# Kernel optimization log

Hardware: AMD Instinct MI355X
Metric: run time of the kernel (lower is better)

## Reference

```python
import jax, jax.numpy as jnp
import numpy as np

D_MODEL = 40; N_LAYER = 256
D_INNER = 80; D_STATE = 16; D_CONV = 4; DT_RANK = 3  # mamba defaults: expand=2, dt_rank=ceil(40/16)
PE_HID = 48; FF_MULT = 4
B, L, N = 1, 400, 65536


def setup_inputs():
    key = jax.random.key(0)
    ks = jax.random.split(key, 16)
    f32 = jnp.float32
    def rn(k, shape, s=0.02):
        return jax.random.normal(k, shape, f32) * s
    inp = {}
    inp['mash_params'] = jax.random.normal(ks[0], (B, L, D_MODEL), f32)
    inp['qry'] = jax.random.uniform(ks[1], (B, N, 3), f32, -1.0, 1.0)
    # stacked per-layer Mamba params (leading dim = N_LAYER)
    inp['l_norm_w'] = jnp.ones((N_LAYER, D_MODEL), f32)
    inp['l_in_w'] = rn(ks[2], (N_LAYER, 2 * D_INNER, D_MODEL), 0.05)
    inp['l_conv_w'] = rn(ks[3], (N_LAYER, D_INNER, D_CONV), 0.2)
    inp['l_conv_b'] = jnp.zeros((N_LAYER, D_INNER), f32)
    inp['l_xproj_w'] = rn(ks[4], (N_LAYER, DT_RANK + 2 * D_STATE, D_INNER), 0.05)
    inp['l_dt_w'] = rn(ks[5], (N_LAYER, D_INNER, DT_RANK), 0.2)
    inp['l_dt_b'] = rn(ks[6], (N_LAYER, D_INNER), 0.5) - 4.0  # softplus -> small dt
    A = jnp.tile(jnp.arange(1, D_STATE + 1, dtype=f32)[None, None, :], (N_LAYER, D_INNER, 1))
    inp['l_A_log'] = jnp.log(A)
    inp['l_D'] = jnp.ones((N_LAYER, D_INNER), f32)
    inp['l_out_w'] = rn(ks[7], (N_LAYER, D_MODEL, D_INNER), 0.05)
    # PointEmbed MLP (Fourier basis is a fixed buffer, built in forward)
    inp['pe_mlp_w'] = rn(ks[8], (D_MODEL, PE_HID + 3), 0.1)
    inp['pe_mlp_b'] = jnp.zeros((D_MODEL,), f32)
    # PreNorm cross-attention (heads=1, dim_head=d_model)
    inp['ca_lnq_w'] = jnp.ones((D_MODEL,), f32); inp['ca_lnq_b'] = jnp.zeros((D_MODEL,), f32)
    inp['ca_lnc_w'] = jnp.ones((D_MODEL,), f32); inp['ca_lnc_b'] = jnp.zeros((D_MODEL,), f32)
    inp['ca_q_w'] = rn(ks[9], (D_MODEL, D_MODEL), 0.1)
    inp['ca_kv_w'] = rn(ks[10], (2 * D_MODEL, D_MODEL), 0.1)
    inp['ca_out_w'] = rn(ks[11], (D_MODEL, D_MODEL), 0.1)
    inp['ca_out_b'] = jnp.zeros((D_MODEL,), f32)
    # PreNorm GEGLU feed-forward
    inp['ff_ln_w'] = jnp.ones((D_MODEL,), f32); inp['ff_ln_b'] = jnp.zeros((D_MODEL,), f32)
    inp['ff_fc1_w'] = rn(ks[12], (2 * FF_MULT * D_MODEL, D_MODEL), 0.1)
    inp['ff_fc1_b'] = jnp.zeros((2 * FF_MULT * D_MODEL,), f32)
    inp['ff_fc2_w'] = rn(ks[13], (D_MODEL, FF_MULT * D_MODEL), 0.1)
    inp['ff_fc2_b'] = jnp.zeros((D_MODEL,), f32)
    inp['out_w'] = rn(ks[14], (1, D_MODEL), 0.1)
    inp['out_b'] = jnp.zeros((1,), f32)
    return inp


def _rmsnorm(x, w, eps=1e-5):
    return x * jax.lax.rsqrt(jnp.mean(x * x, -1, keepdims=True) + eps) * w


def _layernorm(x, w, b, eps=1e-5):
    m = jnp.mean(x, -1, keepdims=True)
    v = jnp.mean((x - m) ** 2, -1, keepdims=True)
    return (x - m) * jax.lax.rsqrt(v + eps) * w + b


def _mamba(u, p):
    # u: [b, l, d_model]
    xz = jnp.einsum('bld,ed->ble', u, p['in_w'])  # [b,l,2*di]
    x, z = jnp.split(xz, 2, -1)
    # depthwise causal conv1d, kernel D_CONV
    xt = jnp.swapaxes(x, 1, 2)  # [b, di, l]
    xc = jax.lax.conv_general_dilated(xt, p['conv_w'][:, None, :], (1,), [(D_CONV - 1, 0)],
                                      feature_group_count=D_INNER)
    x = jax.nn.silu(jnp.swapaxes(xc + p['conv_b'][None, :, None], 1, 2))  # [b,l,di]
    dbc = jnp.einsum('bld,ed->ble', x, p['xproj_w'])  # [b,l,dt_rank+2*ds]
    dtr = dbc[..., :DT_RANK]
    Bm = dbc[..., DT_RANK:DT_RANK + D_STATE]
    Cm = dbc[..., DT_RANK + D_STATE:]
    dt = jax.nn.softplus(jnp.einsum('blr,dr->bld', dtr, p['dt_w']) + p['dt_b'])  # [b,l,di]
    A = -jnp.exp(p['A_log'])  # [di, ds]
    dA = jnp.exp(dt[..., None] * A)                          # [b,l,di,ds]
    dBx = dt[..., None] * Bm[:, :, None, :] * x[..., None]   # [b,l,di,ds]
    def step(h, io):
        a, bx = io
        h = a * h + bx
        return h, h
    h0 = jnp.zeros((u.shape[0], D_INNER, D_STATE), u.dtype)
    _, hs = jax.lax.scan(step, h0, (jnp.moveaxis(dA, 1, 0), jnp.moveaxis(dBx, 1, 0)))
    hs = jnp.moveaxis(hs, 0, 1)  # [b,l,di,ds]
    y = jnp.einsum('blds,bls->bld', hs, Cm) + x * p['D']
    y = y * jax.nn.silu(z)
    return jnp.einsum('bld,ed->ble', y, p['out_w'])


def _forward(mash_params, qry, l_norm_w, l_in_w, l_conv_w, l_conv_b, l_xproj_w, l_dt_w, l_dt_b,
             l_A_log, l_D, l_out_w, pe_mlp_w, pe_mlp_b, ca_lnq_w, ca_lnq_b, ca_lnc_w, ca_lnc_b,
             ca_q_w, ca_kv_w, ca_out_w, ca_out_b, ff_ln_w, ff_ln_b, ff_fc1_w, ff_fc1_b,
             ff_fc2_w, ff_fc2_b, out_w, out_b):
    layer_params = dict(norm_w=l_norm_w, in_w=l_in_w, conv_w=l_conv_w, conv_b=l_conv_b,
                        xproj_w=l_xproj_w, dt_w=l_dt_w, dt_b=l_dt_b, A_log=l_A_log,
                        D=l_D, out_w=l_out_w)
    # Block: residual = x; h = RMSNorm(x); h = Mamba(h); then caller does x = h + residual
    def layer_fn(x, p):
        return x + _mamba(_rmsnorm(x, p['norm_w']), p), None
    x, _ = jax.lax.scan(layer_fn, mash_params, layer_params)
    # PointEmbed: Fourier features with fixed block-diagonal basis
    e = (2.0 ** jnp.arange(PE_HID // 6, dtype=jnp.float32)) * jnp.pi  # [8]
    z0 = jnp.zeros_like(e)
    basis = jnp.stack([jnp.concatenate([e, z0, z0]),
                       jnp.concatenate([z0, e, z0]),
                       jnp.concatenate([z0, z0, e])])  # [3, 24]
    proj = jnp.einsum('bnd,de->bne', qry, basis)
    pe = jnp.concatenate([jnp.sin(proj), jnp.cos(proj), qry], -1)  # [b,n,51]
    q_emb = jnp.einsum('bnf,df->bnd', pe, pe_mlp_w) + pe_mlp_b
    # PreNorm cross-attention (1 head, dim_head = d_model)
    qn = _layernorm(q_emb, ca_lnq_w, ca_lnq_b)
    cn = _layernorm(x, ca_lnc_w, ca_lnc_b)
    q = jnp.einsum('bnd,ed->bne', qn, ca_q_w)
    kv = jnp.einsum('bld,ed->ble', cn, ca_kv_w)
    k, v = jnp.split(kv, 2, -1)
    scale = D_MODEL ** -0.5
    attn = jax.nn.softmax(jnp.einsum('bnd,bld->bnl', q, k) * scale, axis=-1)  # [b,n,l]
    lat = jnp.einsum('bnl,bld->bnd', attn, v)
    lat = jnp.einsum('bnd,ed->bne', lat, ca_out_w) + ca_out_b
    # PreNorm GEGLU feed-forward with residual
    h = _layernorm(lat, ff_ln_w, ff_ln_b)
    a = jnp.einsum('bnd,ed->bne', h, ff_fc1_w) + ff_fc1_b
    x1, g = jnp.split(a, 2, -1)
    ff = jnp.einsum('bnf,df->bnd', x1 * jax.nn.gelu(g, approximate=False), ff_fc2_w) + ff_fc2_b
    lat = lat + ff
    occ = (jnp.einsum('bnd,od->bno', lat, out_w) + out_b)[..., 0]  # [b, n]
    return occ


def reference(mash_params, qry, l_norm_w, l_in_w, l_conv_w, l_conv_b, l_xproj_w, l_dt_w, l_dt_b,
              l_A_log, l_D, l_out_w, pe_mlp_w, pe_mlp_b, ca_lnq_w, ca_lnq_b, ca_lnc_w, ca_lnc_b,
              ca_q_w, ca_kv_w, ca_out_w, ca_out_b, ff_ln_w, ff_ln_b, ff_fc1_w, ff_fc1_b,
              ff_fc2_w, ff_fc2_b, out_w, out_b):
    return _forward(mash_params, qry, l_norm_w, l_in_w, l_conv_w, l_conv_b, l_xproj_w, l_dt_w,
                    l_dt_b, l_A_log, l_D, l_out_w, pe_mlp_w, pe_mlp_b, ca_lnq_w, ca_lnq_b,
                    ca_lnc_w, ca_lnc_b, ca_q_w, ca_kv_w, ca_out_w, ca_out_b, ff_ln_w, ff_ln_b,
                    ff_fc1_w, ff_fc1_b, ff_fc2_w, ff_fc2_b, out_w, out_b)
```

## Files before the change

kernel.cpp:

```cpp
#include <hip/hip_runtime.h>


#define CH 4
#define NCHUNK 100
#define TPB1 320

typedef unsigned long long u64;

__device__ __forceinline__ u64 pack2(float a, float b) {
  return ((u64)__float_as_uint(b) << 32) | (u64)__float_as_uint(a);
}
__device__ __forceinline__ float unplo(u64 a) {
  return __uint_as_float((unsigned)a);
}
__device__ __forceinline__ float unphi(u64 a) {
  return __uint_as_float((unsigned)(a >> 32));
}

__global__ void init_flags(int* __restrict__ flags) {
  int i = blockIdx.x * 256 + threadIdx.x;
  if (i < 256 * 16) flags[i] = 0;
}

__global__ __launch_bounds__(TPB1) void mamba_pipe(
    const float* __restrict__ mash,
    const float* __restrict__ g_norm_w,
    const float* __restrict__ g_in_w,
    const float* __restrict__ g_conv_w,
    const float* __restrict__ g_conv_b,
    const float* __restrict__ g_xp_w,
    const float* __restrict__ g_dt_w,
    const float* __restrict__ g_dt_b,
    const float* __restrict__ g_alog,
    const float* __restrict__ g_D,
    const float* __restrict__ g_out_w,
    float* __restrict__ xb0,
    float* __restrict__ xb1,
    int* __restrict__ flags,
    const float* __restrict__ qry,
    const float* __restrict__ pe_w, const float* __restrict__ pe_b,
    const float* __restrict__ lnq_w, const float* __restrict__ lnq_b,
    const float* __restrict__ qw,
    float* __restrict__ qstore)
{
  const int tid = threadIdx.x;

  if (blockIdx.x >= 256) {
    const int n = (blockIdx.x - 256) * TPB1 + tid;
    if (n < 65536) {
      const float qx = qry[n * 3 + 0], qy = qry[n * 3 + 1], qz = qry[n * 3 + 2];
      float qe[40];
#pragma unroll
      for (int d = 0; d < 40; ++d) qe[d] = pe_b[d];
#pragma unroll 1
      for (int j = 0; j < 8; ++j) {
        float f = 3.14159265358979323846f * (float)(1 << j);
        float sx, cx, sy, cy, sz, cz;
        __sincosf(qx * f, &sx, &cx);
        __sincosf(qy * f, &sy, &cy);
        __sincosf(qz * f, &sz, &cz);
#pragma unroll
        for (int d = 0; d < 40; ++d) {
          const float* r = pe_w + d * 51;
          qe[d] += sx * r[j] + sy * r[j + 8] + sz * r[j + 16]
                 + cx * r[j + 24] + cy * r[j + 32] + cz * r[j + 40];
        }
      }
#pragma unroll
      for (int d = 0; d < 40; ++d) {
        const float* r = pe_w + d * 51;
        qe[d] += qx * r[48] + qy * r[49] + qz * r[50];
      }
      float qn[40];
      {
        float m = 0.f;
#pragma unroll
        for (int d = 0; d < 40; ++d) m += qe[d];
        m *= (1.f / 40.f);
        float var = 0.f;
#pragma unroll
        for (int d = 0; d < 40; ++d) { float dv = qe[d] - m; var += dv * dv; }
        float rstd = rsqrtf(var * (1.f / 40.f) + 1e-5f);
#pragma unroll
        for (int d = 0; d < 40; ++d)
          qn[d] = (qe[d] - m) * rstd * lnq_w[d] + lnq_b[d];
      }
      float q[40];
#pragma unroll
      for (int e = 0; e < 40; ++e) {
        const float* r = qw + e * 40;
        float s = 0.f;
#pragma unroll
        for (int d = 0; d < 40; ++d) s += qn[d] * r[d];
        q[e] = s;
      }
#pragma unroll
      for (int e = 0; e < 40; ++e) qstore[e * 65536 + n] = q[e];
    }
    return;
  }

  const int layer = blockIdx.x;

  __shared__ float xin[160];
  __shared__ float xz[640];
  __shared__ float xs[320];
  __shared__ float dbc[144];
  __shared__ float yb[320];
  __shared__ float xhist[240];

  const int e_in = tid % 160;
  const int tA = tid / 160;
  float w_in_r[40];
  {
    const float4* g = (const float4*)(g_in_w + layer * 6400 + e_in * 40);
    const float4* nw = (const float4*)(g_norm_w + layer * 40);
#pragma unroll
    for (int k = 0; k < 10; ++k) {
      float4 v = g[k];
      float4 n = nw[k];
      w_in_r[4 * k] = v.x * n.x; w_in_r[4 * k + 1] = v.y * n.y;
      w_in_r[4 * k + 2] = v.z * n.z; w_in_r[4 * k + 3] = v.w * n.w;
    }
  }
  const int d_c = tid % 80;
  const int t_c = tid / 80;
  float cw[4]; float cb;
  {
    float4 v = *(const float4*)(g_conv_w + layer * 320 + d_c * 4);
    cw[0] = v.x; cw[1] = v.y; cw[2] = v.z; cw[3] = v.w;
    cb = g_conv_b[layer * 80 + d_c];
  }
  const int halfp = tid & 1;
  const int p_x = tid >> 1;
  const int t_x = p_x / 35, e_x = p_x % 35;
  float w_xp_r[40];
  if (p_x < 140) {
    const float4* g = (const float4*)(g_xp_w + layer * 2800 + e_x * 80 + halfp * 40);
#pragma unroll
    for (int k = 0; k < 10; ++k) {
      float4 v = g[k];
      w_xp_r[4 * k] = v.x; w_xp_r[4 * k + 1] = v.y;
      w_xp_r[4 * k + 2] = v.z; w_xp_r[4 * k + 3] = v.w;
    }
  }
  const int d_ch = tid >> 2;
  const int qq = tid & 3;
  float negA[4], hst[4];
  {
    float4 v = *(const float4*)(g_alog + layer * 1280 + tid * 4);
    negA[0] = -__expf(v.x); negA[1] = -__expf(v.y);
    negA[2] = -__expf(v.z); negA[3] = -__expf(v.w);
    hst[0] = hst[1] = hst[2] = hst[3] = 0.f;
  }
  const float dtw0 = g_dt_w[layer * 240 + d_ch * 3 + 0];
  const float dtw1 = g_dt_w[layer * 240 + d_ch * 3 + 1];
  const float dtw2 = g_dt_w[layer * 240 + d_ch * 3 + 2];
  const float dtb = g_dt_b[layer * 80 + d_ch];
  const float wD = g_D[layer * 80 + d_ch];
  const int p_o = tid >> 1;
  const int t_o = p_o / 40, e_o = p_o % 40;
  float w_out_r[40];
  {
    const float4* g = (const float4*)(g_out_w + layer * 3200 + e_o * 80 + halfp * 40);
#pragma unroll
    for (int k = 0; k < 10; ++k) {
      float4 v = g[k];
      w_out_r[4 * k] = v.x; w_out_r[4 * k + 1] = v.y;
      w_out_r[4 * k + 2] = v.z; w_out_r[4 * k + 3] = v.w;
    }
  }

  for (int i = tid; i < 240; i += TPB1) xhist[i] = 0.f;
  __syncthreads();

  const float* src = (layer == 0) ? mash : ((layer & 1) ? xb0 : xb1);
  float* dst = (layer & 1) ? xb1 : xb0;
  int* flag_prev = flags + (layer - 1) * 16;
  int* flag_cur = flags + layer * 16;

  for (int c = 0; c < NCHUNK; ++c) {
    const int t0 = c * CH;

    if (layer == 0) {
#pragma unroll
      for (int tt = 0; tt < 2; ++tt) {
        const int t = tA + 2 * tt;
        const float4* sp = (const float4*)(src + (t0 + t) * 40);
        float ss = 0.f, sd = 0.f;
#pragma unroll
        for (int k = 0; k < 10; ++k) {
          float4 v = sp[k];
          ss += v.x * v.x + v.y * v.y + v.z * v.z + v.w * v.w;
          sd += w_in_r[4 * k] * v.x + w_in_r[4 * k + 1] * v.y
              + w_in_r[4 * k + 2] * v.z + w_in_r[4 * k + 3] * v.w;
        }
        xz[t * 160 + e_in] = sd * rsqrtf(ss * (1.f / 40.f) + 1e-5f);
      }
      if (tid < 160) xin[tid] = src[t0 * 40 + tid];
    } else {
      while (__hip_atomic_load(flag_prev, __ATOMIC_RELAXED,
                               __HIP_MEMORY_SCOPE_AGENT) <= c)
        __builtin_amdgcn_s_sleep(1);
#pragma unroll
      for (int tt = 0; tt < 2; ++tt) {
        const int t = tA + 2 * tt;
        const u64* sp = (const u64*)(src + (t0 + t) * 40);
        float ss = 0.f, sd = 0.f;
#pragma unroll
        for (int k = 0; k < 20; ++k) {
          u64 a = __hip_atomic_load(sp + k, __ATOMIC_RELAXED,
                                    __HIP_MEMORY_SCOPE_AGENT);
          float v0 = unplo(a), v1 = unphi(a);
          ss += v0 * v0 + v1 * v1;
          sd += w_in_r[2 * k] * v0 + w_in_r[2 * k + 1] * v1;
        }
        xz[t * 160 + e_in] = sd * rsqrtf(ss * (1.f / 40.f) + 1e-5f);
      }
      if (tid < 80) {
        u64 a = __hip_atomic_load((const u64*)(src + t0 * 40) + tid,
                                  __ATOMIC_RELAXED, __HIP_MEMORY_SCOPE_AGENT);
        xin[2 * tid] = unplo(a);
        xin[2 * tid + 1] = unphi(a);
      }
    }
    __syncthreads();

    {
      float acc = cb;
#pragma unroll
      for (int j = 0; j < 4; ++j) {
        int lt = t_c - 3 + j;
        float xv = (lt >= 0) ? xz[lt * 160 + d_c] : xhist[(lt + 3) * 80 + d_c];
        acc += cw[j] * xv;
      }
      xs[t_c * 80 + d_c] = acc / (1.f + __expf(-acc));
    }
    __syncthreads();

    if (p_x < 140) {
      const float4* xp = (const float4*)&xs[t_x * 80 + halfp * 40];
      float s = 0.f;
#pragma unroll
      for (int k = 0; k < 10; ++k) {
        float4 v = xp[k];
        s += w_xp_r[4 * k] * v.x + w_xp_r[4 * k + 1] * v.y
           + w_xp_r[4 * k + 2] * v.z + w_xp_r[4 * k + 3] * v.w;
      }
      s += __shfl_xor(s, 1);
      if (halfp == 0) dbc[t_x * 36 + e_x] = s;
    } else {
      for (int k = tid - 280; k < 240; k += 40)
        xhist[k] = xz[(1 + k / 80) * 160 + (k % 80)];
    }
    __syncthreads();

#pragma unroll
    for (int t = 0; t < CH; ++t) {
      const float* db = &dbc[t * 36];
      float sdt = dtb + db[0] * dtw0 + db[1] * dtw1 + db[2] * dtw2;
      float dtval = (sdt > 15.f) ? sdt : __logf(1.f + __expf(sdt));
      float xval = xs[t * 80 + d_ch];
      float part = 0.f;
#pragma unroll
      for (int j = 0; j < 4; ++j) {
        int s_i = qq * 4 + j;
        float Bv = db[3 + s_i];
        float Cv = db[19 + s_i];
        hst[j] = __expf(dtval * negA[j]) * hst[j] + dtval * Bv * xval;
        part += hst[j] * Cv;
      }
      part += __shfl_xor(part, 1);
      part += __shfl_xor(part, 2);
      if (qq == 0) {
        float yv = part + xval * wD;
        float z = xz[t * 160 + 80 + d_ch];
        yb[t * 80 + d_ch] = yv * z / (1.f + __expf(-z));
      }
    }
    __syncthreads();

    {
      const float4* yp = (const float4*)&yb[t_o * 80 + halfp * 40];
      float s = 0.f;
#pragma unroll
      for (int k = 0; k < 10; ++k) {
        float4 v = yp[k];
        s += w_out_r[4 * k] * v.x + w_out_r[4 * k + 1] * v.y
           + w_out_r[4 * k + 2] * v.z + w_out_r[4 * k + 3] * v.w;
      }
      s += __shfl_xor(s, 1);
      float r = xin[p_o] + s;
      float r2 = __shfl_xor(r, 2);
      if ((tid & 3) == 0)
        __hip_atomic_store((u64*)(dst + t0 * 40 + p_o), pack2(r, r2),
                           __ATOMIC_RELAXED, __HIP_MEMORY_SCOPE_AGENT);
    }
    __syncthreads();
    if (tid == 0)
      __hip_atomic_store(flag_cur, c + 1, __ATOMIC_RELAXED,
                         __HIP_MEMORY_SCOPE_AGENT);
  }
}

__global__ __launch_bounds__(64) void kv_kernel(
    const float* __restrict__ xfin,
    const float* __restrict__ lnc_w, const float* __restrict__ lnc_b,
    const float* __restrict__ kv_w,
    float* __restrict__ kbuf, float* __restrict__ vbuf)
{
  int t = blockIdx.x;
  int lane = threadIdx.x;
  float x = (lane < 40) ? xfin[t * 40 + lane] : 0.f;
  float s = x;
#pragma unroll
  for (int o = 32; o >= 1; o >>= 1) s += __shfl_xor(s, o);
  float m = s * (1.f / 40.f);
  float dv = (lane < 40) ? (x - m) : 0.f;
  float v2 = dv * dv;
#pragma unroll
  for (int o = 32; o >= 1; o >>= 1) v2 += __shfl_xor(v2, o);
  float rstd = rsqrtf(v2 * (1.f / 40.f) + 1e-5f);
  __shared__ float cn[40];
  if (lane < 40) cn[lane] = dv * rstd * lnc_w[lane] + lnc_b[lane];
  __syncthreads();
  for (int e = lane; e < 80; e += 64) {
    float acc = 0.f;
#pragma unroll
    for (int d = 0; d < 40; ++d) acc += cn[d] * kv_w[e * 40 + d];
    if (e < 40) kbuf[t * 40 + e] = acc;
    else vbuf[t * 40 + (e - 40)] = acc;
  }
}

__global__ __launch_bounds__(256) void query_fast(
    const float* __restrict__ qstore,
    const float* __restrict__ ow, const float* __restrict__ ob,
    const float* __restrict__ flw, const float* __restrict__ flb,
    const float* __restrict__ w1, const float* __restrict__ b1,
    const float* __restrict__ w2, const float* __restrict__ b2,
    const float* __restrict__ outw, const float* __restrict__ outb,
    const float* __restrict__ kbuf, const float* __restrict__ vbuf,
    float* __restrict__ out)
{
  const int tid = threadIdx.x;
  const int h = __builtin_amdgcn_readfirstlane((tid >> 6) & 3);
  const int lane = tid & 63;
  const int n = blockIdx.x * 64 + lane;
  const int p1 = tid ^ 64, p2 = tid ^ 128, p3 = tid ^ 192;
  __shared__ float colbuf[40 * 256];

  float q[40];
#pragma unroll
  for (int e = 0; e < 40; ++e) q[e] = qstore[e * 65536 + n];

  float acc[40];
#pragma unroll
  for (int d = 0; d < 40; ++d) acc[d] = 0.f;
  float mx = -1e30f, l = 0.f;
  const float scale = 0.15811388300841897f;
  const int tbeg = h * 100;
#pragma unroll 1
  for (int t = tbeg; t < tbeg + 100; t += 2) {
    const float4* ka = (const float4*)(kbuf + t * 40);
    const float4* kb = (const float4*)(kbuf + t * 40 + 40);
    float a0 = 0.f, a1 = 0.f, b0 = 0.f, b1s = 0.f;
#pragma unroll
    for (int k = 0; k < 10; ++k) {
      float4 k4 = ka[k];
      float4 j4 = kb[k];
      a0 += q[4 * k] * k4.x + q[4 * k + 1] * k4.y;
      a1 += q[4 * k + 2] * k4.z + q[4 * k + 3] * k4.w;
      b0 += q[4 * k] * j4.x + q[4 * k + 1] * j4.y;
      b1s += q[4 * k + 2] * j4.z + q[4 * k + 3] * j4.w;
    }
    float sa = (a0 + a1) * scale;
    float sb = (b0 + b1s) * scale;
    {
      if (sa > mx) {
        float corr = __expf(mx - sa);
        l *= corr;
#pragma unroll
        for (int d = 0; d < 40; ++d) acc[d] *= corr;
        mx = sa;
      }
      float p = __expf(sa - mx);
      l += p;
      const float4* vr = (const float4*)(vbuf + t * 40);
#pragma unroll
      for (int k = 0; k < 10; ++k) {
        float4 v4 = vr[k];
        acc[4 * k] += p * v4.x; acc[4 * k + 1] += p * v4.y;
        acc[4 * k + 2] += p * v4.z; acc[4 * k + 3] += p * v4.w;
      }
    }
    {
      if (sb > mx) {
        float corr = __expf(mx - sb);
        l *= corr;
#pragma unroll
        for (int d = 0; d < 40; ++d) acc[d] *= corr;
        mx = sb;
      }
      float p = __expf(sb - mx);
      l += p;
      const float4* vr = (const float4*)(vbuf + (t + 1) * 40);
#pragma unroll
      for (int k = 0; k < 10; ++k) {
        float4 v4 = vr[k];
        acc[4 * k] += p * v4.x; acc[4 * k + 1] += p * v4.y;
        acc[4 * k + 2] += p * v4.z; acc[4 * k + 3] += p * v4.w;
      }
    }
  }

  {
    float* redm = colbuf;
    float* redl = colbuf + 256;
    redm[tid] = mx; redl[tid] = l;
  }
  __syncthreads();
  float a0c, a1c, a2c, a3c, linv;
  {
    float m1 = colbuf[p1], m2 = colbuf[p2], m3 = colbuf[p3];
    float l1 = colbuf[256 + p1], l2 = colbuf[256 + p2], l3 = colbuf[256 + p3];
    float nm = fmaxf(fmaxf(mx, m1), fmaxf(m2, m3));
    a0c = __expf(mx - nm); a1c = __expf(m1 - nm);
    a2c = __expf(m2 - nm); a3c = __expf(m3 - nm);
    float L = l * a0c + l1 * a1c + l2 * a2c + l3 * a3c;
    linv = 1.f / L;
  }
  __syncthreads();
#pragma unroll
  for (int d = 0; d < 40; ++d) colbuf[d * 256 + tid] = acc[d];
  __syncthreads();
  float lat[40];
#pragma unroll
  for (int d = 0; d < 40; ++d)
    lat[d] = (acc[d] * a0c + colbuf[d * 256 + p1] * a1c
            + colbuf[d * 256 + p2] * a2c + colbuf[d * 256 + p3] * a3c) * linv;
  __syncthreads();

  float lath[10];
#pragma unroll
  for (int dd = 0; dd < 10; ++dd) {
    float v = lat[dd];
    v = (h == 1) ? lat[dd + 10] : v;
    v = (h == 2) ? lat[dd + 20] : v;
    v = (h == 3) ? lat[dd + 30] : v;
    lath[dd] = v;
  }
  float lp[40];
#pragma unroll
  for (int e = 0; e < 40; ++e) lp[e] = 0.f;
#pragma unroll 1
  for (int dd = 0; dd < 10; ++dd) {
    const float lv = lath[dd];
    const int d = h * 10 + dd;
#pragma unroll
    for (int e = 0; e < 40; ++e) lp[e] += lv * ow[e * 40 + d];
  }
#pragma unroll
  for (int e = 0; e < 40; ++e) colbuf[e * 256 + tid] = lp[e];
  __syncthreads();
  float lat2[40];
#pragma unroll
  for (int e = 0; e < 40; ++e)
    lat2[e] = ob[e] + lp[e] + colbuf[e * 256 + p1]
            + colbuf[e * 256 + p2] + colbuf[e * 256 + p3];
  __syncthreads();

  float hh[40];
  {
    float m = 0.f;
#pragma unroll
    for (int d = 0; d < 40; ++d) m += lat2[d];
    m *= (1.f / 40.f);
    float var = 0.f;
#pragma unroll
    for (int d = 0; d < 40; ++d) { float dv = lat2[d] - m; var += dv * dv; }
    float rstd = rsqrtf(var * (1.f / 40.f) + 1e-5f);
#pragma unroll
    for (int d = 0; d < 40; ++d) hh[d] = (lat2[d] - m) * rstd * flw[d] + flb[d];
  }
  float ff[40];
#pragma unroll
  for (int d = 0; d < 40; ++d) ff[d] = 0.f;
#pragma unroll 1
  for (int ee = 0; ee < 40; ++ee) {
    const int e = h * 40 + ee;
    const float* r1 = w1 + e * 40;
    const float* r2 = w1 + (160 + e) * 40;
    float s0 = 0.f, s1 = 0.f;
#pragma unroll
    for (int d = 0; d < 40; ++d) { s0 += hh[d] * r1[d]; s1 += hh[d] * r2[d]; }
    float x1 = s0 + b1[e];
    float g = s1 + b1[160 + e];
    float tv = x1 * (0.5f * g * (1.f + erff(g * 0.70710678118654752f)));
#pragma unroll
    for (int d = 0; d < 40; ++d) ff[d] += tv * w2[d * 160 + e];
  }
#pragma unroll
  for (int d = 0; d < 40; ++d) colbuf[d * 256 + tid] = ff[d];
  __syncthreads();
  float r = outb[0];
#pragma unroll
  for (int d = 0; d < 40; ++d) {
    float f = ff[d] + colbuf[d * 256 + p1] + colbuf[d * 256 + p2]
            + colbuf[d * 256 + p3] + b2[d];
    r += (lat2[d] + f) * outw[d];
  }
  if (h == 0) out[n] = r;
}

__global__ __launch_bounds__(256) void query_kernel_fb(
    const float* __restrict__ qry,
    const float* __restrict__ pe_w, const float* __restrict__ pe_b,
    const float* __restrict__ lnq_w, const float* __restrict__ lnq_b,
    const float* __restrict__ qw,
    const float* __restrict__ ow, const float* __restrict__ ob,
    const float* __restrict__ flw, const float* __restrict__ flb,
    const float* __restrict__ w1, const float* __restrict__ b1,
    const float* __restrict__ w2, const float* __restrict__ b2,
    const float* __restrict__ outw, const float* __restrict__ outb,
    const float* __restrict__ kbuf, const float* __restrict__ vbuf,
    float* __restrict__ out)
{
  const int tid = threadIdx.x;
  const int h = __builtin_amdgcn_readfirstlane((tid >> 6) & 1);
  const int pj = tid >> 7;
  const int lane = tid & 63;
  const int n = blockIdx.x * 128 + pj * 64 + lane;
  const int ptn = tid ^ 64;
  __shared__ float colbuf[40 * 256];
  __shared__ float redm[256], redl[256];

  const float qx = qry[n * 3 + 0], qy = qry[n * 3 + 1], qz = qry[n * 3 + 2];
  float qp[40];
#pragma unroll
  for (int d = 0; d < 40; ++d) qp[d] = 0.f;
#pragma unroll
  for (int jj = 0; jj < 4; ++jj) {
    const int j = h * 4 + jj;
    float f = 3.14159265358979323846f * (float)(1 << j);
    float sx, cx, sy, cy, sz, cz;
    __sincosf(qx * f, &sx, &cx);
    __sincosf(qy * f, &sy, &cy);
    __sincosf(qz * f, &sz, &cz);
#pragma unroll
    for (int d = 0; d < 40; ++d) {
      const float* r = pe_w + d * 51;
      qp[d] += sx * r[j] + sy * r[j + 8] + sz * r[j + 16]
             + cx * r[j + 24] + cy * r[j + 32] + cz * r[j + 40];
    }
  }
#pragma unroll
  for (int d = 0; d < 40; ++d) colbuf[d * 256 + tid] = qp[d];
  __syncthreads();
  float qe[40];
#pragma unroll
  for (int d = 0; d < 40; ++d) {
    const float* r = pe_w + d * 51;
    qe[d] = pe_b[d] + qp[d] + colbuf[d * 256 + ptn]
          + qx * r[48] + qy * r[49] + qz * r[50];
  }
  __syncthreads();
  float qn[40];
  {
    float m = 0.f;
#pragma unroll
    for (int d = 0; d < 40; ++d) m += qe[d];
    m *= (1.f / 40.f);
    float var = 0.f;
#pragma unroll
    for (int d = 0; d < 40; ++d) { float dv = qe[d] - m; var += dv * dv; }
    float rstd = rsqrtf(var * (1.f / 40.f) + 1e-5f);
#pragma unroll
    for (int d = 0; d < 40; ++d) qn[d] = (qe[d] - m) * rstd * lnq_w[d] + lnq_b[d];
  }
  float qnh[20];
#pragma unroll
  for (int dd = 0; dd < 20; ++dd) qnh[dd] = h ? qn[dd + 20] : qn[dd];
  float q[40];
#pragma unroll
  for (int e = 0; e < 40; ++e) q[e] = 0.f;
#pragma unroll 1
  for (int dd = 0; dd < 20; ++dd) {
    const float qv = qnh[dd];
    const int d = h * 20 + dd;
#pragma unroll
    for (int e = 0; e < 40; ++e) q[e] += qv * qw[e * 40 + d];
  }
#pragma unroll
  for (int e = 0; e < 40; ++e) colbuf[e * 256 + tid] = q[e];
  __syncthreads();
#pragma unroll
  for (int e = 0; e < 40; ++e) q[e] += colbuf[e * 256 + ptn];
  __syncthreads();

  float acc[40];
#pragma unroll
  for (int d = 0; d < 40; ++d) acc[d] = 0.f;
  float mx = -1e30f, l = 0.f;
  const float scale = 0.15811388300841897f;
  const int tbeg = h * 200, tend = tbeg + 200;
#pragma unroll 1
  for (int t = tbeg; t < tend; ++t) {
    const float4* kr = (const float4*)(kbuf + t * 40);
    float s0 = 0.f, s1 = 0.f, s2 = 0.f, s3 = 0.f;
#pragma unroll
    for (int k = 0; k < 10; ++k) {
      float4 k4 = kr[k];
      s0 += q[4 * k] * k4.x; s1 += q[4 * k + 1] * k4.y;
      s2 += q[4 * k + 2] * k4.z; s3 += q[4 * k + 3] * k4.w;
    }
    float s = ((s0 + s1) + (s2 + s3)) * scale;
    if (s > mx) {
      float corr = __expf(mx - s);
      l *= corr;
#pragma unroll
      for (int d = 0; d < 40; ++d) acc[d] *= corr;
      mx = s;
    }
    float p = __expf(s - mx);
    l += p;
    const float4* vr = (const float4*)(vbuf + t * 40);
#pragma unroll
    for (int k = 0; k < 10; ++k) {
      float4 v4 = vr[k];
      acc[4 * k] += p * v4.x; acc[4 * k + 1] += p * v4.y;
      acc[4 * k + 2] += p * v4.z; acc[4 * k + 3] += p * v4.w;
    }
  }
#pragma unroll
  for (int d = 0; d < 40; ++d) colbuf[d * 256 + tid] = acc[d];
  redm[tid] = mx; redl[tid] = l;
  __syncthreads();
  float lat[40];
  {
    float m2 = redm[ptn];
    float l2 = redl[ptn];
    float nm = fmaxf(mx, m2);
    float a = __expf(mx - nm), b = __expf(m2 - nm);
    float lm = l * a + l2 * b;
    float linv = 1.f / lm;
#pragma unroll
    for (int d = 0; d < 40; ++d)
      lat[d] = (acc[d] * a + colbuf[d * 256 + ptn] * b) * linv;
  }
  __syncthreads();
  float lath[20];
#pragma unroll
  for (int dd = 0; dd < 20; ++dd) lath[dd] = h ? lat[dd + 20] : lat[dd];
  float lp[40];
#pragma unroll
  for (int e = 0; e < 40; ++e) lp[e] = 0.f;
#pragma unroll 1
  for (int dd = 0; dd < 20; ++dd) {
    const float lv = lath[dd];
    const int d = h * 20 + dd;
#pragma unroll
    for (int e = 0; e < 40; ++e) lp[e] += lv * ow[e * 40 + d];
  }
#pragma unroll
  for (int e = 0; e < 40; ++e) colbuf[e * 256 + tid] = lp[e];
  __syncthreads();
  float lat2[40];
#pragma unroll
  for (int e = 0; e < 40; ++e) lat2[e] = ob[e] + lp[e] + colbuf[e * 256 + ptn];
  __syncthreads();
  float hh[40];
  {
    float m = 0.f;
#pragma unroll
    for (int d = 0; d < 40; ++d) m += lat2[d];
    m *= (1.f / 40.f);
    float var = 0.f;
#pragma unroll
    for (int d = 0; d < 40; ++d) { float dv = lat2[d] - m; var += dv * dv; }
    float rstd = rsqrtf(var * (1.f / 40.f) + 1e-5f);
#pragma unroll
    for (int d = 0; d < 40; ++d) hh[d] = (lat2[d] - m) * rstd * flw[d] + flb[d];
  }
  float ff[40];
#pragma unroll
  for (int d = 0; d < 40; ++d) ff[d] = 0.f;
#pragma unroll 1
  for (int ee = 0; ee < 80; ++ee) {
    const int e = h * 80 + ee;
    const float* r1 = w1 + e * 40;
    const float* r2 = w1 + (160 + e) * 40;
    float s0 = 0.f, s1 = 0.f;
#pragma unroll
    for (int d = 0; d < 40; ++d) { s0 += hh[d] * r1[d]; s1 += hh[d] * r2[d]; }
    float x1 = s0 + b1[e];
    float g = s1 + b1[160 + e];
    float tv = x1 * (0.5f * g * (1.f + erff(g * 0.70710678118654752f)));
#pragma unroll
    for (int d = 0; d < 40; ++d) ff[d] += tv * w2[d * 160 + e];
  }
#pragma unroll
  for (int d = 0; d < 40; ++d) colbuf[d * 256 + tid] = ff[d];
  __syncthreads();
  float r = outb[0];
#pragma unroll
  for (int d = 0; d < 40; ++d) {
    float f = ff[d] + colbuf[d * 256 + ptn] + b2[d];
    r += (lat2[d] + f) * outw[d];
  }
  if (h == 0) out[n] = r;
}

extern "C" void kernel_launch(void* const* d_in, const int* in_sizes, int n_in,
                              void* d_out, int out_size, void* d_ws, size_t ws_size,
                              hipStream_t stream) {
  const float* mash   = (const float*)d_in[0];
  const float* qry    = (const float*)d_in[1];
  const float* lnw    = (const float*)d_in[2];
  const float* linw   = (const float*)d_in[3];
  const float* lconvw = (const float*)d_in[4];
  const float* lconvb = (const float*)d_in[5];
  const float* lxpw   = (const float*)d_in[6];
  const float* ldtw   = (const float*)d_in[7];
  const float* ldtb   = (const float*)d_in[8];
  const float* lAlog  = (const float*)d_in[9];
  const float* lD     = (const float*)d_in[10];
  const float* loutw  = (const float*)d_in[11];
  const float* pew    = (const float*)d_in[12];
  const float* peb    = (const float*)d_in[13];
  const float* lnqw   = (const float*)d_in[14];
  const float* lnqb   = (const float*)d_in[15];
  const float* lncw   = (const float*)d_in[16];
  const float* lncb   = (const float*)d_in[17];
  const float* qw     = (const float*)d_in[18];
  const float* kvw    = (const float*)d_in[19];
  const float* oww    = (const float*)d_in[20];
  const float* owb    = (const float*)d_in[21];
  const float* flnw   = (const float*)d_in[22];
  const float* flnb   = (const float*)d_in[23];
  const float* w1     = (const float*)d_in[24];
  const float* b1     = (const float*)d_in[25];
  const float* w2     = (const float*)d_in[26];
  const float* b2     = (const float*)d_in[27];
  const float* outw   = (const float*)d_in[28];
  const float* outb   = (const float*)d_in[29];

  float* wsf = (float*)d_ws;
  float* xb0 = wsf;
  float* xb1 = wsf + 16000;
  float* kbuf = wsf + 32000;
  float* vbuf = wsf + 48000;
  int* flags = (int*)(wsf + 64000);
  float* qstore = wsf + 68096;
  const size_t needed = (size_t)68096 * 4 + (size_t)40 * 65536 * 4;
  const bool pre = ws_size >= needed;

  hipLaunchKernelGGL(init_flags, dim3(16), dim3(256), 0, stream, flags);
  hipLaunchKernelGGL(mamba_pipe, dim3(pre ? 461 : 256), dim3(TPB1), 0, stream,
                     mash, lnw, linw, lconvw, lconvb, lxpw, ldtw, ldtb, lAlog,
                     lD, loutw, xb0, xb1, flags,
                     qry, pew, peb, lnqw, lnqb, qw, qstore);
  hipLaunchKernelGGL(kv_kernel, dim3(400), dim3(64), 0, stream,
                     xb1, lncw, lncb, kvw, kbuf, vbuf);
  if (pre) {
    hipLaunchKernelGGL(query_fast, dim3(1024), dim3(256), 0, stream,
                       qstore, oww, owb, flnw, flnb,
                       w1, b1, w2, b2, outw, outb, kbuf, vbuf, (float*)d_out);
  } else {
    hipLaunchKernelGGL(query_kernel_fb, dim3(512), dim3(256), 0, stream,
                       qry, pew, peb, lnqw, lnqb, qw, oww, owb, flnw, flnb,
                       w1, b1, w2, b2, outw, outb, kbuf, vbuf, (float*)d_out);
  }
}
```

Baseline: 2.113 ms.

## Pack two consecutive Mamba layers per block with shared-memory handoff

Each pipeline block now holds two layers as two 320-thread groups, so 128 blocks cover the 256 layers. The second group runs one chunk behind the first and reads its output from a double-buffered shared array instead of through global atomics and flags. This halves the cross-block flag and polling handoffs along the serial layer chain. In exchange, both groups advance in lockstep under shared barriers with one extra skew iteration. The block size rises to 640 threads, which also applies to the point-embedding blocks and may limit registers per thread.

```diff
diff --git a/kernel.cpp b/kernel.cpp
--- a/kernel.cpp
+++ b/kernel.cpp
@@ -3,7 +3,8 @@
 
 #define CH 4
 #define NCHUNK 100
-#define TPB1 320
+#define TPB1 640
+#define NLB 128
 
 typedef unsigned long long u64;
 
@@ -45,8 +46,8 @@
 {
   const int tid = threadIdx.x;
 
-  if (blockIdx.x >= 256) {
-    const int n = (blockIdx.x - 256) * TPB1 + tid;
+  if (blockIdx.x >= NLB) {
+    const int n = (blockIdx.x - NLB) * TPB1 + tid;
     if (n < 65536) {
       const float qx = qry[n * 3 + 0], qy = qry[n * 3 + 1], qz = qry[n * 3 + 2];
       float qe[40];
@@ -100,55 +101,59 @@
     return;
   }
 
-  const int layer = blockIdx.x;
-
-  __shared__ float xin[160];
-  __shared__ float xz[640];
-  __shared__ float xs[320];
-  __shared__ float dbc[144];
-  __shared__ float yb[320];
-  __shared__ float xhist[240];
-
-  const int e_in = tid % 160;
-  const int tA = tid / 160;
+  const int blk = blockIdx.x;
+  const int g = tid / 320;
+  const int ltid = tid - g * 320;
+  const int layer = 2 * blk + g;
+
+  __shared__ float xz[2][640];
+  __shared__ float xs[2][320];
+  __shared__ float dbc[2][144];
+  __shared__ float yb[2][320];
+  __shared__ float xhist[2][240];
+  __shared__ float ho[2][160];
+  __shared__ float xin0[160];
+
+  const int e_in = ltid % 160;
+  const int tA = ltid / 160;
   float w_in_r[40];
   {
-    const float4* g = (const float4*)(g_in_w + layer * 6400 + e_in * 40);
+    const float4* gg = (const float4*)(g_in_w + layer * 6400 + e_in * 40);
     const float4* nw = (const float4*)(g_norm_w + layer * 40);
 #pragma unroll
     for (int k = 0; k < 10; ++k) {
-      float4 v = g[k];
+      float4 v = gg[k];
       float4 n = nw[k];
       w_in_r[4 * k] = v.x * n.x; w_in_r[4 * k + 1] = v.y * n.y;
       w_in_r[4 * k + 2] = v.z * n.z; w_in_r[4 * k + 3] = v.w * n.w;
     }
   }
-  const int d_c = tid % 80;
-  const int t_c = tid / 80;
+  const int d_c = ltid % 80;
+  const int t_c = ltid / 80;
   float cw[4]; float cb;
   {
     float4 v = *(const float4*)(g_conv_w + layer * 320 + d_c * 4);
     cw[0] = v.x; cw[1] = v.y; cw[2] = v.z; cw[3] = v.w;
     cb = g_conv_b[layer * 80 + d_c];
   }
-  const int halfp = tid & 1;
-  const int p_x = tid >> 1;
+  const int halfp = ltid & 1;
+  const int p_x = ltid >> 1;
   const int t_x = p_x / 35, e_x = p_x % 35;
   float w_xp_r[40];
   if (p_x < 140) {
-    const float4* g = (const float4*)(g_xp_w + layer * 2800 + e_x * 80 + halfp * 40);
+    const float4* gg = (const float4*)(g_xp_w + layer * 2800 + e_x * 80 + halfp * 40);
 #pragma unroll
     for (int k = 0; k < 10; ++k) {
-      float4 v = g[k];
+      float4 v = gg[k];
       w_xp_r[4 * k] = v.x; w_xp_r[4 * k + 1] = v.y;
       w_xp_r[4 * k + 2] = v.z; w_xp_r[4 * k + 3] = v.w;
     }
   }
-  const int d_ch = tid >> 2;
-  const int qq = tid & 3;
+  const int d_ch = ltid >> 2;
+  const int qq = ltid & 3;
   float negA[4], hst[4];
   {
-    float4 v = *(const float4*)(g_alog + layer * 1280 + tid * 4);
+    float4 v = *(const float4*)(g_alog + layer * 1280 + ltid * 4);
     negA[0] = -__expf(v.x); negA[1] = -__expf(v.y);
     negA[2] = -__expf(v.z); negA[3] = -__expf(v.w);
     hst[0] = hst[1] = hst[2] = hst[3] = 0.f;
@@ -158,35 +163,82 @@
   const float dtw2 = g_dt_w[layer * 240 + d_ch * 3 + 2];
   const float dtb = g_dt_b[layer * 80 + d_ch];
   const float wD = g_D[layer * 80 + d_ch];
-  const int p_o = tid >> 1;
+  const int p_o = ltid >> 1;
   const int t_o = p_o / 40, e_o = p_o % 40;
   float w_out_r[40];
   {
-    const float4* g = (const float4*)(g_out_w + layer * 3200 + e_o * 80 + halfp * 40);
+    const float4* gg = (const float4*)(g_out_w + layer * 3200 + e_o * 80 + halfp * 40);
 #pragma unroll
     for (int k = 0; k < 10; ++k) {
-      float4 v = g[k];
+      float4 v = gg[k];
       w_out_r[4 * k] = v.x; w_out_r[4 * k + 1] = v.y;
       w_out_r[4 * k + 2] = v.z; w_out_r[4 * k + 3] = v.w;
     }
   }
 
-  for (int i = tid; i < 240; i += TPB1) xhist[i] = 0.f;
-  __syncthreads();
-
-  const float* src = (layer == 0) ? mash : ((layer & 1) ? xb0 : xb1);
-  float* dst = (layer & 1) ? xb1 : xb0;
-  int* flag_prev = flags + (layer - 1) * 16;
-  int* flag_cur = flags + layer * 16;
-
-  for (int c = 0; c < NCHUNK; ++c) {
+  for (int i = ltid; i < 240; i += 320) xhist[g][i] = 0.f;
+  __syncthreads();
+
+  const float* src = (blk == 0) ? mash : ((blk & 1) ? xb0 : xb1);
+  float* dst = (blk & 1) ? xb1 : xb0;
+  int* flag_prev = flags + (blk - 1) * 16;
+  int* flag_cur = flags + blk * 16;
+
+  for (int i = 0; i <= NCHUNK; ++i) {
+    const bool act0 = (g == 0) && (i < NCHUNK);
+    const bool act1 = (g == 1) && (i >= 1);
+    const int c = (g == 0) ? i : (i - 1);
     const int t0 = c * CH;
-
-    if (layer == 0) {
+    const int hb = c & 1;
+
+    if (act0) {
+      if (blk == 0) {
+#pragma unroll
+        for (int tt = 0; tt < 2; ++tt) {
+          const int t = tA + 2 * tt;
+          const float4* sp = (const float4*)(src + (t0 + t) * 40);
+          float ss = 0.f, sd = 0.f;
+#pragma unroll
+          for (int k = 0; k < 10; ++k) {
+            float4 v = sp[k];
+            ss += v.x * v.x + v.y * v.y + v.z * v.z + v.w * v.w;
+            sd += w_in_r[4 * k] * v.x + w_in_r[4 * k + 1] * v.y
+                + w_in_r[4 * k + 2] * v.z + w_in_r[4 * k + 3] * v.w;
+          }
+          xz[0][t * 160 + e_in] = sd * rsqrtf(ss * (1.f / 40.f) + 1e-5f);
+        }
+        if (ltid < 160) xin0[ltid] = src[t0 * 40 + ltid];
+      } else {
+        while (__hip_atomic_load(flag_prev, __ATOMIC_RELAXED,
+                                 __HIP_MEMORY_SCOPE_AGENT) <= i)
+          __builtin_amdgcn_s_sleep(1);
+#pragma unroll
+        for (int tt = 0; tt < 2; ++tt) {
+          const int t = tA + 2 * tt;
+          const u64* sp = (const u64*)(src + (t0 + t) * 40);
+          float ss = 0.f, sd = 0.f;
+#pragma unroll
+          for (int k = 0; k < 20; ++k) {
+            u64 a = __hip_atomic_load(sp + k, __ATOMIC_RELAXED,
+                                      __HIP_MEMORY_SCOPE_AGENT);
+            float v0 = unplo(a), v1 = unphi(a);
+            ss += v0 * v0 + v1 * v1;
+            sd += w_in_r[2 * k] * v0 + w_in_r[2 * k + 1] * v1;
+          }
+          xz[0][t * 160 + e_in] = sd * rsqrtf(ss * (1.f / 40.f) + 1e-5f);
+        }
+        if (ltid < 80) {
+          u64 a = __hip_atomic_load((const u64*)(src + t0 * 40) + ltid,
+                                    __ATOMIC_RELAXED, __HIP_MEMORY_SCOPE_AGENT);
+          xin0[2 * ltid] = unplo(a);
+          xin0[2 * ltid + 1] = unphi(a);
+        }
+      }
+    } else if (act1) {
 #pragma unroll
       for (int tt = 0; tt < 2; ++tt) {
         const int t = tA + 2 * tt;
-        const float4* sp = (const float4*)(src + (t0 + t) * 40);
+        const float4* sp = (const float4*)&ho[hb][t * 40];
         float ss = 0.f, sd = 0.f;
 #pragma unroll
         for (int k = 0; k < 10; ++k) {
@@ -195,93 +247,72 @@
           sd += w_in_r[4 * k] * v.x + w_in_r[4 * k + 1] * v.y
               + w_in_r[4 * k + 2] * v.z + w_in_r[4 * k + 3] * v.w;
         }
-        xz[t * 160 + e_in] = sd * rsqrtf(ss * (1.f / 40.f) + 1e-5f);
-      }
-      if (tid < 160) xin[tid] = src[t0 * 40 + tid];
-    } else {
-      while (__hip_atomic_load(flag_prev, __ATOMIC_RELAXED,
-                               __HIP_MEMORY_SCOPE_AGENT) <= c)
-        __builtin_amdgcn_s_sleep(1);
-#pragma unroll
-      for (int tt = 0; tt < 2; ++tt) {
-        const int t = tA + 2 * tt;
-        const u64* sp = (const u64*)(src + (t0 + t) * 40);
-        float ss = 0.f, sd = 0.f;
-#pragma unroll
-        for (int k = 0; k < 20; ++k) {
-          u64 a = __hip_atomic_load(sp + k, __ATOMIC_RELAXED,
-                                    __HIP_MEMORY_SCOPE_AGENT);
-          float v0 = unplo(a), v1 = unphi(a);
-          ss += v0 * v0 + v1 * v1;
-          sd += w_in_r[2 * k] * v0 + w_in_r[2 * k + 1] * v1;
-        }
-        xz[t * 160 + e_in] = sd * rsqrtf(ss * (1.f / 40.f) + 1e-5f);
-      }
-      if (tid < 80) {
-        u64 a = __hip_atomic_load((const u64*)(src + t0 * 40) + tid,
-                                  __ATOMIC_RELAXED, __HIP_MEMORY_SCOPE_AGENT);
-        xin[2 * tid] = unplo(a);
-        xin[2 * tid + 1] = unphi(a);
+        xz[1][t * 160 + e_in] = sd * rsqrtf(ss * (1.f / 40.f) + 1e-5f);
       }
     }
     __syncthreads();
 
-    {
+    if (act0 || act1) {
       float acc = cb;
 #pragma unroll
       for (int j = 0; j < 4; ++j) {
         int lt = t_c - 3 + j;
-        float xv = (lt >= 0) ? xz[lt * 160 + d_c] : xhist[(lt + 3) * 80 + d_c];
+        float xv = (lt >= 0) ? xz[g][lt * 160 + d_c]
+                             : xhist[g][(lt + 3) * 80 + d_c];
         acc += cw[j] * xv;
       }
-      xs[t_c * 80 + d_c] = acc / (1.f + __expf(-acc));
+      xs[g][t_c * 80 + d_c] = acc / (1.f + __expf(-acc));
     }
     __syncthreads();
 
-    if (p_x < 140) {
-      const float4* xp = (const float4*)&xs[t_x * 80 + halfp * 40];
-      float s = 0.f;
-#pragma unroll
-      for (int k = 0; k < 10; ++k) {
-        float4 v = xp[k];
-        s += w_xp_r[4 * k] * v.x + w_xp_r[4 * k + 1] * v.y
-           + w_xp_r[4 * k + 2] * v.z + w_xp_r[4 * k + 3] * v.w;
-      }
-      s += __shfl_xor(s, 1);
-      if (halfp == 0) dbc[t_x * 36 + e_x] = s;
-    } else {
-      for (int k = tid - 280; k < 240; k += 40)
-        xhist[k] = xz[(1 + k / 80) * 160 + (k % 80)];
+    if (act0 || act1) {
+      if (p_x < 140) {
+        const float4* xp = (const float4*)&xs[g][t_x * 80 + halfp * 40];
+        float s = 0.f;
+#pragma unroll
+        for (int k = 0; k < 10; ++k) {
+          float4 v = xp[k];
+          s += w_xp_r[4 * k] * v.x + w_xp_r[4 * k + 1] * v.y
+             + w_xp_r[4 * k + 2] * v.z + w_xp_r[4 * k + 3] * v.w;
+        }
+        s += __shfl_xor(s, 1);
+        if (halfp == 0) dbc[g][t_x * 36 + e_x] = s;
+      } else {
+        for (int k = ltid - 280; k < 240; k += 40)
+          xhist[g][k] = xz[g][(1 + k / 80) * 160 + (k % 80)];
+      }
     }
     __syncthreads();
 
-#pragma unroll
-    for (int t = 0; t < CH; ++t) {
-      const float* db = &dbc[t * 36];
-      float sdt = dtb + db[0] * dtw0 + db[1] * dtw1 + db[2] * dtw2;
-      float dtval = (sdt > 15.f) ? sdt : __logf(1.f + __expf(sdt));
-      float xval = xs[t * 80 + d_ch];
-      float part = 0.f;
-#pragma unroll
-      for (int j = 0; j < 4; ++j) {
-        int s_i = qq * 4 + j;
-        float Bv = db[3 + s_i];
-        float Cv = db[19 + s_i];
-        hst[j] = __expf(dtval * negA[j]) * hst[j] + dtval * Bv * xval;
-        part += hst[j] * Cv;
-      }
-      part += __shfl_xor(part, 1);
-      part += __shfl_xor(part, 2);
-      if (qq == 0) {
-        float yv = part + xval * wD;
-        float z = xz[t * 160 + 80 + d_ch];
-        yb[t * 80 + d_ch] = yv * z / (1.f + __expf(-z));
+    if (act0 || act1) {
+#pragma unroll
+      for (int t = 0; t < CH; ++t) {
+        const float* db = &dbc[g][t * 36];
+        float sdt = dtb + db[0] * dtw0 + db[1] * dtw1 + db[2] * dtw2;
+        float dtval = (sdt > 15.f) ? sdt : __logf(1.f + __expf(sdt));
+        float xval = xs[g][t * 80 + d_ch];
+        float part = 0.f;
+#pragma unroll
+        for (int j = 0; j < 4; ++j) {
+          int s_i = qq * 4 + j;
+          float Bv = db[3 + s_i];
+          float Cv = db[19 + s_i];
+          hst[j] = __expf(dtval * negA[j]) * hst[j] + dtval * Bv * xval;
+          part += hst[j] * Cv;
+        }
+        part += __shfl_xor(part, 1);
+        part += __shfl_xor(part, 2);
+        if (qq == 0) {
+          float yv = part + xval * wD;
+          float z = xz[g][t * 160 + 80 + d_ch];
+          yb[g][t * 80 + d_ch] = yv * z / (1.f + __expf(-z));
+        }
       }
     }
     __syncthreads();
 
-    {
-      const float4* yp = (const float4*)&yb[t_o * 80 + halfp * 40];
+    if (act0) {
+      const float4* yp = (const float4*)&yb[0][t_o * 80 + halfp * 40];
       float s = 0.f;
 #pragma unroll
       for (int k = 0; k < 10; ++k) {
@@ -290,14 +321,25 @@
            + w_out_r[4 * k + 2] * v.z + w_out_r[4 * k + 3] * v.w;
       }
       s += __shfl_xor(s, 1);
-      float r = xin[p_o] + s;
+      if (halfp == 0) ho[hb][p_o] = xin0[p_o] + s;
+    } else if (act1) {
+      const float4* yp = (const float4*)&yb[1][t_o * 80 + halfp * 40];
+      float s = 0.f;
+#pragma unroll
+      for (int k = 0; k < 10; ++k) {
+        float4 v = yp[k];
+        s += w_out_r[4 * k] * v.x + w_out_r[4 * k + 1] * v.y
+           + w_out_r[4 * k + 2] * v.z + w_out_r[4 * k + 3] * v.w;
+      }
+      s += __shfl_xor(s, 1);
+      float r = ho[hb][p_o] + s;
       float r2 = __shfl_xor(r, 2);
-      if ((tid & 3) == 0)
+      if ((ltid & 3) == 0)
         __hip_atomic_store((u64*)(dst + t0 * 40 + p_o), pack2(r, r2),
                            __ATOMIC_RELAXED, __HIP_MEMORY_SCOPE_AGENT);
     }
     __syncthreads();
-    if (tid == 0)
+    if (act1 && ltid == 0)
       __hip_atomic_store(flag_cur, c + 1, __ATOMIC_RELAXED,
                          __HIP_MEMORY_SCOPE_AGENT);
   }
@@ -756,7 +798,9 @@
   const bool pre = ws_size >= needed;
 
   hipLaunchKernelGGL(init_flags, dim3(16), dim3(256), 0, stream, flags);
-  hipLaunchKernelGGL(mamba_pipe, dim3(pre ? 461 : 256), dim3(TPB1), 0, stream,
+  const int npe = (65536 + TPB1 - 1) / TPB1;
+  hipLaunchKernelGGL(mamba_pipe, dim3(pre ? NLB + npe : NLB), dim3(TPB1), 0,
+                     stream,
                      mash, lnw, linw, lconvw, lconvb, lxpw, ldtw, ldtb, lAlog,
                      lD, loutw, xb0, xb1, flags,
                      qry, pew, peb, lnqw, lnqb, qw, qstore);
```

Result: slower. 4.636 ms (+119.5%).

## Halve Mamba pipeline chunk size and keep conv history in registers

Applied to the files above, without the earlier changes.

The layer-pipelined Mamba kernel now processes two timesteps per chunk instead of four, doubling the number of chunks. This lowers the startup latency of the wavefront across 256 layer blocks. The causal conv history moves from shared memory into per-thread registers, and one __syncthreads per chunk is removed by fusing the in-projection and conv stages. The cost is twice as many flag handoffs between layers and less work per thread in each stage.

```diff
diff --git a/kernel.cpp b/kernel.cpp
--- a/kernel.cpp
+++ b/kernel.cpp
@@ -1,8 +1,8 @@
 #include <hip/hip_runtime.h>
 
 
-#define CH 4
-#define NCHUNK 100
+#define CH 2
+#define NCHUNK 200
 #define TPB1 320
 
 typedef unsigned long long u64;
@@ -102,18 +102,15 @@
 
   const int layer = blockIdx.x;
 
-  __shared__ float xin[160];
-  __shared__ float xz[640];
-  __shared__ float xs[320];
-  __shared__ float dbc[144];
-  __shared__ float yb[320];
-  __shared__ float xhist[240];
-
-  const int e_in = tid % 160;
-  const int tA = tid / 160;
+  __shared__ float xs[2][80];
+  __shared__ float zb[2][80];
+  __shared__ float dbc[2][36];
+  __shared__ float yb[2][80];
+  __shared__ float xin0[80];
+
   float w_in_r[40];
-  {
-    const float4* g = (const float4*)(g_in_w + layer * 6400 + e_in * 40);
+  if (tid < 160) {
+    const float4* g = (const float4*)(g_in_w + layer * 6400 + tid * 40);
     const float4* nw = (const float4*)(g_norm_w + layer * 40);
 #pragma unroll
     for (int k = 0; k < 10; ++k) {
@@ -123,19 +120,18 @@
       w_in_r[4 * k + 2] = v.z * n.z; w_in_r[4 * k + 3] = v.w * n.w;
     }
   }
-  const int d_c = tid % 80;
-  const int t_c = tid / 80;
-  float cw[4]; float cb;
-  {
-    float4 v = *(const float4*)(g_conv_w + layer * 320 + d_c * 4);
-    cw[0] = v.x; cw[1] = v.y; cw[2] = v.z; cw[3] = v.w;
-    cb = g_conv_b[layer * 80 + d_c];
+  float cw0, cw1, cw2, cw3, cb;
+  float h0 = 0.f, h1 = 0.f, h2 = 0.f;
+  if (tid < 80) {
+    float4 v = *(const float4*)(g_conv_w + layer * 320 + tid * 4);
+    cw0 = v.x; cw1 = v.y; cw2 = v.z; cw3 = v.w;
+    cb = g_conv_b[layer * 80 + tid];
   }
   const int halfp = tid & 1;
   const int p_x = tid >> 1;
   const int t_x = p_x / 35, e_x = p_x % 35;
   float w_xp_r[40];
-  if (p_x < 140) {
+  if (p_x < 70) {
     const float4* g = (const float4*)(g_xp_w + layer * 2800 + e_x * 80 + halfp * 40);
 #pragma unroll
     for (int k = 0; k < 10; ++k) {
@@ -161,7 +157,7 @@
   const int p_o = tid >> 1;
   const int t_o = p_o / 40, e_o = p_o % 40;
   float w_out_r[40];
-  {
+  if (p_o < 80) {
     const float4* g = (const float4*)(g_out_w + layer * 3200 + e_o * 80 + halfp * 40);
 #pragma unroll
     for (int k = 0; k < 10; ++k) {
@@ -170,8 +166,6 @@
       w_out_r[4 * k + 2] = v.z; w_out_r[4 * k + 3] = v.w;
     }
   }
-
-  for (int i = tid; i < 240; i += TPB1) xhist[i] = 0.f;
   __syncthreads();
 
   const float* src = (layer == 0) ? mash : ((layer & 1) ? xb0 : xb1);
@@ -182,64 +176,67 @@
   for (int c = 0; c < NCHUNK; ++c) {
     const int t0 = c * CH;
 
+    float xzv0 = 0.f, xzv1 = 0.f;
     if (layer == 0) {
-#pragma unroll
-      for (int tt = 0; tt < 2; ++tt) {
-        const int t = tA + 2 * tt;
-        const float4* sp = (const float4*)(src + (t0 + t) * 40);
-        float ss = 0.f, sd = 0.f;
-#pragma unroll
-        for (int k = 0; k < 10; ++k) {
-          float4 v = sp[k];
-          ss += v.x * v.x + v.y * v.y + v.z * v.z + v.w * v.w;
-          sd += w_in_r[4 * k] * v.x + w_in_r[4 * k + 1] * v.y
-              + w_in_r[4 * k + 2] * v.z + w_in_r[4 * k + 3] * v.w;
+      if (tid < 160) {
+#pragma unroll
+        for (int t = 0; t < 2; ++t) {
+          const float4* sp = (const float4*)(src + (t0 + t) * 40);
+          float ss = 0.f, sd = 0.f;
+#pragma unroll
+          for (int k = 0; k < 10; ++k) {
+            float4 v = sp[k];
+            ss += v.x * v.x + v.y * v.y + v.z * v.z + v.w * v.w;
+            sd += w_in_r[4 * k] * v.x + w_in_r[4 * k + 1] * v.y
+                + w_in_r[4 * k + 2] * v.z + w_in_r[4 * k + 3] * v.w;
+          }
+          float v = sd * rsqrtf(ss * (1.f / 40.f) + 1e-5f);
+          if (t == 0) xzv0 = v; else xzv1 = v;
         }
-        xz[t * 160 + e_in] = sd * rsqrtf(ss * (1.f / 40.f) + 1e-5f);
-      }
-      if (tid < 160) xin[tid] = src[t0 * 40 + tid];
+      } else if (tid < 240) {
+        xin0[tid - 160] = src[t0 * 40 + (tid - 160)];
+      }
     } else {
       while (__hip_atomic_load(flag_prev, __ATOMIC_RELAXED,
                                __HIP_MEMORY_SCOPE_AGENT) <= c)
         __builtin_amdgcn_s_sleep(1);
-#pragma unroll
-      for (int tt = 0; tt < 2; ++tt) {
-        const int t = tA + 2 * tt;
-        const u64* sp = (const u64*)(src + (t0 + t) * 40);
-        float ss = 0.f, sd = 0.f;
-#pragma unroll
-        for (int k = 0; k < 20; ++k) {
-          u64 a = __hip_atomic_load(sp + k, __ATOMIC_RELAXED,
-                                    __HIP_MEMORY_SCOPE_AGENT);
-          float v0 = unplo(a), v1 = unphi(a);
-          ss += v0 * v0 + v1 * v1;
-          sd += w_in_r[2 * k] * v0 + w_in_r[2 * k + 1] * v1;
+      if (tid < 160) {
+#pragma unroll
+        for (int t = 0; t < 2; ++t) {
+          const u64* sp = (const u64*)(src + (t0 + t) * 40);
+          float ss = 0.f, sd = 0.f;
+#pragma unroll
+          for (int k = 0; k < 20; ++k) {
+            u64 a = __hip_atomic_load(sp + k, __ATOMIC_RELAXED,
+                                      __HIP_MEMORY_SCOPE_AGENT);
+            float v0 = unplo(a), v1 = unphi(a);
+            ss += v0 * v0 + v1 * v1;
+            sd += w_in_r[2 * k] * v0 + w_in_r[2 * k + 1] * v1;
+          }
+          float v = sd * rsqrtf(ss * (1.f / 40.f) + 1e-5f);
+          if (t == 0) xzv0 = v; else xzv1 = v;
         }
-        xz[t * 160 + e_in] = sd * rsqrtf(ss * (1.f / 40.f) + 1e-5f);
-      }
-      if (tid < 80) {
-        u64 a = __hip_atomic_load((const u64*)(src + t0 * 40) + tid,
+      } else if (tid < 200) {
+        u64 a = __hip_atomic_load((const u64*)(src + t0 * 40) + (tid - 160),
                                   __ATOMIC_RELAXED, __HIP_MEMORY_SCOPE_AGENT);
-        xin[2 * tid] = unplo(a);
-        xin[2 * tid + 1] = unphi(a);
-      }
+        xin0[2 * (tid - 160)] = unplo(a);
+        xin0[2 * (tid - 160) + 1] = unphi(a);
+      }
+    }
+    if (tid < 80) {
+      float c0 = cb + cw0 * h0 + cw1 * h1 + cw2 * h2 + cw3 * xzv0;
+      float c1 = cb + cw0 * h1 + cw1 * h2 + cw2 * xzv0 + cw3 * xzv1;
+      xs[0][tid] = c0 / (1.f + __expf(-c0));
+      xs[1][tid] = c1 / (1.f + __expf(-c1));
+      h0 = h2; h1 = xzv0; h2 = xzv1;
+    } else if (tid < 160) {
+      zb[0][tid - 80] = xzv0;
+      zb[1][tid - 80] = xzv1;
     }
     __syncthreads();
 
-    {
-      float acc = cb;
-#pragma unroll
-      for (int j = 0; j < 4; ++j) {
-        int lt = t_c - 3 + j;
-        float xv = (lt >= 0) ? xz[lt * 160 + d_c] : xhist[(lt + 3) * 80 + d_c];
-        acc += cw[j] * xv;
-      }
-      xs[t_c * 80 + d_c] = acc / (1.f + __expf(-acc));
-    }
-    __syncthreads();
-
-    if (p_x < 140) {
-      const float4* xp = (const float4*)&xs[t_x * 80 + halfp * 40];
+    if (p_x < 70) {
+      const float4* xp = (const float4*)&xs[t_x][halfp * 40];
       float s = 0.f;
 #pragma unroll
       for (int k = 0; k < 10; ++k) {
@@ -248,19 +245,16 @@
            + w_xp_r[4 * k + 2] * v.z + w_xp_r[4 * k + 3] * v.w;
       }
       s += __shfl_xor(s, 1);
-      if (halfp == 0) dbc[t_x * 36 + e_x] = s;
-    } else {
-      for (int k = tid - 280; k < 240; k += 40)
-        xhist[k] = xz[(1 + k / 80) * 160 + (k % 80)];
+      if (halfp == 0) dbc[t_x][e_x] = s;
     }
     __syncthreads();
 
 #pragma unroll
     for (int t = 0; t < CH; ++t) {
-      const float* db = &dbc[t * 36];
+      const float* db = &dbc[t][0];
       float sdt = dtb + db[0] * dtw0 + db[1] * dtw1 + db[2] * dtw2;
       float dtval = (sdt > 15.f) ? sdt : __logf(1.f + __expf(sdt));
-      float xval = xs[t * 80 + d_ch];
+      float xval = xs[t][d_ch];
       float part = 0.f;
 #pragma unroll
       for (int j = 0; j < 4; ++j) {
@@ -274,14 +268,14 @@
       part += __shfl_xor(part, 2);
       if (qq == 0) {
         float yv = part + xval * wD;
-        float z = xz[t * 160 + 80 + d_ch];
-        yb[t * 80 + d_ch] = yv * z / (1.f + __expf(-z));
+        float z = zb[t][d_ch];
+        yb[t][d_ch] = yv * z / (1.f + __expf(-z));
       }
     }
     __syncthreads();
 
-    {
-      const float4* yp = (const float4*)&yb[t_o * 80 + halfp * 40];
+    if (p_o < 80) {
+      const float4* yp = (const float4*)&yb[t_o][halfp * 40];
       float s = 0.f;
 #pragma unroll
       for (int k = 0; k < 10; ++k) {
@@ -290,7 +284,7 @@
            + w_out_r[4 * k + 2] * v.z + w_out_r[4 * k + 3] * v.w;
       }
       s += __shfl_xor(s, 1);
-      float r = xin[p_o] + s;
+      float r = xin0[p_o] + s;
       float r2 = __shfl_xor(r, 2);
       if ((tid & 3) == 0)
         __hip_atomic_store((u64*)(dst + t0 * 40 + p_o), pack2(r, r2),
```

After: 2.678 ms. 1.27x slower.
